# Optimization experiments

Hardware: AMD Instinct MI355X
Metric: run time of the kernel (lower is better)

Reference implementation:

```python
import jax, jax.numpy as jnp
import numpy as np

TEMPERATURE = 0.5

def setup_inputs() -> dict:
    key = jax.random.key(0)
    k1, k2 = jax.random.split(key)
    z_i = jax.random.normal(k1, (4096, 128), dtype=jnp.float32)
    z_j = jax.random.normal(k2, (4096, 128), dtype=jnp.float32)
    return {"z_i": z_i, "z_j": z_j}

def reference(z_i, z_j):
    n = z_i.shape[0]
    # L2 normalize each view (eps matches torch F.normalize default 1e-12)
    def l2norm(x):
        return x / jnp.maximum(jnp.linalg.norm(x, axis=1, keepdims=True), 1e-12)
    z = jnp.concatenate([l2norm(z_i), l2norm(z_j)], axis=0)  # [2N, D]
    sim = (z @ z.T) / TEMPERATURE                             # [2N, 2N]
    m = 2 * n
    idx = jnp.arange(m)
    pos_idx = jnp.concatenate([jnp.arange(n, m), jnp.arange(n)])  # positive pair index
    pos = sim[idx, pos_idx]                                   # [2N]
    # Per original: logits = [pos] ++ (row with diagonal removed); positive thus
    # appears twice in the logsumexp. Mask diagonal with -inf, prepend pos column.
    neg_inf = jnp.finfo(sim.dtype).min
    sim_masked = jnp.where(idx[:, None] == idx[None, :], neg_inf, sim)
    logits = jnp.concatenate([pos[:, None], sim_masked], axis=1)  # [2N, 2N+1]
    lse = jax.nn.logsumexp(logits, axis=1)
    loss = jnp.mean(lse - pos)
    return loss
```

## Files before the change

kernel.cpp:

```cpp
#include <hip/hip_runtime.h>
#include <hip/hip_bf16.h>

#define M_ROWS 8192
#define HALF_N 4096
#define D 128
#define INV_T 2.0f
#define NT 4

typedef __attribute__((ext_vector_type(4))) float f32x4;
typedef __attribute__((ext_vector_type(8))) short bf16x8;
typedef unsigned int u32;
typedef __attribute__((ext_vector_type(4))) u32 u32x4;

__global__ __launch_bounds__(256) void k_normalize(
    const float* __restrict__ zi, const float* __restrict__ zj,
    __hip_bfloat16* __restrict__ zb, float* __restrict__ rowsum)
{
    int t = blockIdx.x * 256 + threadIdx.x;
    if (t < M_ROWS) rowsum[t] = 0.0f;

    int row  = t >> 6;
    int lane = t & 63;
    const float* src = (row < HALF_N) ? (zi + (size_t)row * D)
                                      : (zj + (size_t)(row - HALF_N) * D);
    float2 v = *(const float2*)(src + lane * 2);
    float ss = v.x * v.x + v.y * v.y;
    #pragma unroll
    for (int o = 32; o >= 1; o >>= 1) ss += __shfl_xor(ss, o);
    float scale = 1.0f / fmaxf(sqrtf(ss), 1e-12f);

    __hip_bfloat162 o2;
    o2.x = __float2bfloat16(v.x * scale);
    o2.y = __float2bfloat16(v.y * scale);
    *(__hip_bfloat162*)(zb + (size_t)row * D + lane * 2) = o2;
}

__global__ __launch_bounds__(256, 2) void k_simsum(
    const __hip_bfloat16* __restrict__ zb, float* __restrict__ rowsum)
{
    __shared__ char sB[2][32768];

    const int ibase  = blockIdx.y * 128;
    const int chunk  = blockIdx.x;
    const int jbase0 = chunk * (NT * 128);
    const int tid    = threadIdx.x;
    const int wv     = tid >> 6, lane = tid & 63;
    const int lr     = lane & 15, lg = lane >> 4;
    const int rbase  = wv * 32;

    bf16x8 a[2][4];
    #pragma unroll
    for (int m = 0; m < 2; ++m)
        #pragma unroll
        for (int ks = 0; ks < 4; ++ks) {
            int row = ibase + rbase + m * 16 + lr;
            a[m][ks] = *(const bf16x8*)(zb + (size_t)row * D + (ks * 4 + lg) * 8);
        }

    u32x4 breg[8];
    auto load_tile = [&](int t) {
        int jb = jbase0 + t * 128;
        #pragma unroll
        for (int i = 0; i < 8; ++i) {
            int row = (wv * 8 + i) * 4 + lg;
            breg[i] = *(const u32x4*)(zb + (size_t)(jb + row) * D + lr * 8);
        }
    };
    auto write_tile = [&](char* buf) {
        #pragma unroll
        for (int i = 0; i < 8; ++i) {
            int row = (wv * 8 + i) * 4 + lg;
            *(u32x4*)(buf + row * 256 + ((lr ^ (row & 7)) << 4)) = breg[i];
        }
    };

    float eacc[2][4] = {{0.f, 0.f, 0.f, 0.f}, {0.f, 0.f, 0.f, 0.f}};

    load_tile(0);
    write_tile(sB[0]);
    __syncthreads();

    for (int t = 0; t < NT; ++t) {
        if (t + 1 < NT) load_tile(t + 1);
        const char* cur = sB[t & 1];

        f32x4 acc[2][8];
        #pragma unroll
        for (int m = 0; m < 2; ++m)
            #pragma unroll
            for (int n = 0; n < 8; ++n) acc[m][n] = (f32x4){0.f, 0.f, 0.f, 0.f};

        #pragma unroll
        for (int ks = 0; ks < 4; ++ks) {
            #pragma unroll
            for (int n = 0; n < 8; ++n) {
                int rowB = n * 16 + lr;
                bf16x8 b = *(const bf16x8*)(cur + rowB * 256 +
                            ((((ks << 2) + lg) ^ (lr & 7)) << 4));
                acc[0][n] = __builtin_amdgcn_mfma_f32_16x16x32_bf16(a[0][ks], b, acc[0][n], 0, 0, 0);
                acc[1][n] = __builtin_amdgcn_mfma_f32_16x16x32_bf16(a[1][ks], b, acc[1][n], 0, 0, 0);
            }
        }

        #pragma unroll
        for (int m = 0; m < 2; ++m)
            #pragma unroll
            for (int n = 0; n < 8; ++n)
                #pragma unroll
                for (int r = 0; r < 4; ++r)
                    eacc[m][r] += __expf(INV_T * acc[m][n][r]);

        __syncthreads();
        if (t + 1 < NT) {
            write_tile(sB[(t + 1) & 1]);
            __syncthreads();
        }
    }

    #pragma unroll
    for (int m = 0; m < 2; ++m)
        #pragma unroll
        for (int r = 0; r < 4; ++r) {
            float e = eacc[m][r];
            e += __shfl_xor(e, 1);
            e += __shfl_xor(e, 2);
            e += __shfl_xor(e, 4);
            e += __shfl_xor(e, 8);
            if (lr == 0)
                atomicAdd(&rowsum[ibase + rbase + m * 16 + lg * 4 + r], e);
        }
}

__global__ __launch_bounds__(256) void k_rowloss(
    const __hip_bfloat16* __restrict__ zb, const float* __restrict__ rowsum,
    float* __restrict__ rowloss)
{
    int t = blockIdx.x * 256 + threadIdx.x;
    int row = t >> 6, lane = t & 63;
    int pair = row ^ HALF_N;

    __hip_bfloat162 av = *(const __hip_bfloat162*)(zb + (size_t)row  * D + lane * 2);
    __hip_bfloat162 bv = *(const __hip_bfloat162*)(zb + (size_t)pair * D + lane * 2);
    float ax = __bfloat162float(av.x), ay = __bfloat162float(av.y);
    float bx = __bfloat162float(bv.x), by = __bfloat162float(bv.y);
    float sd = ax * ax + ay * ay;
    float pd = ax * bx + ay * by;
    #pragma unroll
    for (int o = 32; o >= 1; o >>= 1) {
        sd += __shfl_xor(sd, o);
        pd += __shfl_xor(pd, o);
    }
    if (lane == 0) {
        float rs  = rowsum[row];
        float val = rs - __expf(INV_T * sd) + __expf(INV_T * pd);
        rowloss[row] = logf(val) - INV_T * pd;
    }
}

__global__ __launch_bounds__(1024) void k_reduce(
    const float* __restrict__ rowloss, float* __restrict__ out)
{
    __shared__ float sm[16];
    int tid = threadIdx.x;
    float s = 0.f;
    #pragma unroll
    for (int i = 0; i < M_ROWS / 1024; ++i) s += rowloss[i * 1024 + tid];
    #pragma unroll
    for (int o = 32; o >= 1; o >>= 1) s += __shfl_xor(s, o);
    if ((tid & 63) == 0) sm[tid >> 6] = s;
    __syncthreads();
    if (tid == 0) {
        float tot = 0.f;
        #pragma unroll
        for (int w = 0; w < 16; ++w) tot += sm[w];
        out[0] = tot * (1.0f / (float)M_ROWS);
    }
}

extern "C" void kernel_launch(void* const* d_in, const int* in_sizes, int n_in,
                              void* d_out, int out_size, void* d_ws, size_t ws_size,
                              hipStream_t stream)
{
    const float* zi = (const float*)d_in[0];
    const float* zj = (const float*)d_in[1];

    float* rowsum  = (float*)d_ws;
    float* rowloss = rowsum + M_ROWS;
    __hip_bfloat16* zb = (__hip_bfloat16*)((char*)d_ws + 65536);

    k_normalize<<<dim3(M_ROWS * 64 / 256), 256, 0, stream>>>(zi, zj, zb, rowsum);
    k_simsum<<<dim3(16, 64), dim3(256), 0, stream>>>(zb, rowsum);
    k_rowloss<<<dim3(M_ROWS * 64 / 256), 256, 0, stream>>>(zb, rowsum, rowloss);
    k_reduce<<<dim3(1), dim3(1024), 0, stream>>>(rowloss, (float*)d_out);
}
```

Before: 38.77 us.

## Exploit similarity symmetry to compute only upper-triangular tile panels

Uses the symmetry of z·zᵀ so each block computes only tiles with column panel at or after its row panel. Column sums of the exp values are reduced through shared memory and atomically added to the column rows, which roughly halves the MFMA and exp work. The shared-memory tile buffer becomes single-buffered, and occupancy is raised to 3 blocks per SIMD. In exchange it adds extra shuffles, LDS traffic and atomics per tile, and the triangular grid leaves many blocks exiting early and others with fewer tiles, which causes load imbalance.

```diff
diff --git a/kernel.cpp b/kernel.cpp
--- a/kernel.cpp
+++ b/kernel.cpp
@@ -5,7 +5,8 @@
 #define HALF_N 4096
 #define D 128
 #define INV_T 2.0f
-#define NT 4
+#define NTC 4
+#define NPANEL 64
 
 typedef __attribute__((ext_vector_type(4))) float f32x4;
 typedef __attribute__((ext_vector_type(8))) short bf16x8;
@@ -35,18 +36,22 @@
     *(__hip_bfloat162*)(zb + (size_t)row * D + lane * 2) = o2;
 }
 
-__global__ __launch_bounds__(256, 2) void k_simsum(
+__global__ __launch_bounds__(256, 3) void k_simsum(
     const __hip_bfloat16* __restrict__ zb, float* __restrict__ rowsum)
 {
-    __shared__ char sB[2][32768];
-
-    const int ibase  = blockIdx.y * 128;
-    const int chunk  = blockIdx.x;
-    const int jbase0 = chunk * (NT * 128);
-    const int tid    = threadIdx.x;
-    const int wv     = tid >> 6, lane = tid & 63;
-    const int lr     = lane & 15, lg = lane >> 4;
-    const int rbase  = wv * 32;
+    __shared__ char  sB[32768];
+    __shared__ float colLDS[4][128];
+
+    const int pi = blockIdx.y;
+    const int j0 = pi + blockIdx.x * NTC;
+    if (j0 >= NPANEL) return;
+    const int ntiles = min(NTC, NPANEL - j0);
+
+    const int ibase = pi * 128;
+    const int tid   = threadIdx.x;
+    const int wv    = tid >> 6, lane = tid & 63;
+    const int lr    = lane & 15, lg = lane >> 4;
+    const int rbase = wv * 32;
 
     bf16x8 a[2][4];
     #pragma unroll
@@ -58,31 +63,30 @@
         }
 
     u32x4 breg[8];
-    auto load_tile = [&](int t) {
-        int jb = jbase0 + t * 128;
+    auto load_tile = [&](int pj) {
         #pragma unroll
         for (int i = 0; i < 8; ++i) {
             int row = (wv * 8 + i) * 4 + lg;
-            breg[i] = *(const u32x4*)(zb + (size_t)(jb + row) * D + lr * 8);
+            breg[i] = *(const u32x4*)(zb + (size_t)(pj * 128 + row) * D + lr * 8);
         }
     };
-    auto write_tile = [&](char* buf) {
+    auto write_tile = [&]() {
         #pragma unroll
         for (int i = 0; i < 8; ++i) {
             int row = (wv * 8 + i) * 4 + lg;
-            *(u32x4*)(buf + row * 256 + ((lr ^ (row & 7)) << 4)) = breg[i];
+            *(u32x4*)(sB + row * 256 + ((lr ^ (row & 7)) << 4)) = breg[i];
         }
     };
 
     float eacc[2][4] = {{0.f, 0.f, 0.f, 0.f}, {0.f, 0.f, 0.f, 0.f}};
 
-    load_tile(0);
-    write_tile(sB[0]);
+    load_tile(j0);
+    write_tile();
     __syncthreads();
 
-    for (int t = 0; t < NT; ++t) {
-        if (t + 1 < NT) load_tile(t + 1);
-        const char* cur = sB[t & 1];
+    for (int t = 0; t < ntiles; ++t) {
+        const int pj = j0 + t;
+        if (t + 1 < ntiles) load_tile(pj + 1);
 
         f32x4 acc[2][8];
         #pragma unroll
@@ -95,26 +99,43 @@
             #pragma unroll
             for (int n = 0; n < 8; ++n) {
                 int rowB = n * 16 + lr;
-                bf16x8 b = *(const bf16x8*)(cur + rowB * 256 +
+                bf16x8 b = *(const bf16x8*)(sB + rowB * 256 +
                             ((((ks << 2) + lg) ^ (lr & 7)) << 4));
                 acc[0][n] = __builtin_amdgcn_mfma_f32_16x16x32_bf16(a[0][ks], b, acc[0][n], 0, 0, 0);
                 acc[1][n] = __builtin_amdgcn_mfma_f32_16x16x32_bf16(a[1][ks], b, acc[1][n], 0, 0, 0);
             }
         }
 
+        float cs[8] = {0.f, 0.f, 0.f, 0.f, 0.f, 0.f, 0.f, 0.f};
         #pragma unroll
         for (int m = 0; m < 2; ++m)
             #pragma unroll
             for (int n = 0; n < 8; ++n)
                 #pragma unroll
-                for (int r = 0; r < 4; ++r)
-                    eacc[m][r] += __expf(INV_T * acc[m][n][r]);
+                for (int r = 0; r < 4; ++r) {
+                    float e = __expf(INV_T * acc[m][n][r]);
+                    eacc[m][r] += e;
+                    cs[n]      += e;
+                }
+
+        #pragma unroll
+        for (int n = 0; n < 8; ++n) {
+            cs[n] += __shfl_xor(cs[n], 16);
+            cs[n] += __shfl_xor(cs[n], 32);
+        }
+        if (lg == 0) {
+            #pragma unroll
+            for (int n = 0; n < 8; ++n) colLDS[wv][n * 16 + lr] = cs[n];
+        }
 
         __syncthreads();
-        if (t + 1 < NT) {
-            write_tile(sB[(t + 1) & 1]);
-            __syncthreads();
-        }
+        if (t + 1 < ntiles) write_tile();
+        if (pj != pi && tid < 128) {
+            float cv = colLDS[0][tid] + colLDS[1][tid] +
+                       colLDS[2][tid] + colLDS[3][tid];
+            atomicAdd(&rowsum[pj * 128 + tid], cv);
+        }
+        __syncthreads();
     }
 
     #pragma unroll
```

After: 53.19 us. +37.2%, slower.

## Replace atomic row sums with per-chunk partials and deepen the B-tile prefetch

Applied to the files above, without the earlier changes.

Each simsum block now writes its row partial sums to a per-chunk buffer instead of atomically adding, and the rowloss kernel sums the eight partials with its existing shuffle reduction. The grid is halved in x by doubling tiles per block (NT 4→8), which gives better reuse of the A fragments. The LDS pipeline now preloads two tiles ahead and writes the next tile at the top of each iteration, dropping one barrier per iteration. exp is computed as exp2f with a folded constant. Fewer blocks (512) may reduce occupancy and load balance on the GPU.

```diff
diff --git a/kernel.cpp b/kernel.cpp
--- a/kernel.cpp
+++ b/kernel.cpp
@@ -4,8 +4,9 @@
 #define M_ROWS 8192
 #define HALF_N 4096
 #define D 128
-#define INV_T 2.0f
-#define NT 4
+#define NT 8
+#define NCHUNK 8
+#define E2C 2.8853900817779268f
 
 typedef __attribute__((ext_vector_type(4))) float f32x4;
 typedef __attribute__((ext_vector_type(8))) short bf16x8;
@@ -14,11 +15,9 @@
 
 __global__ __launch_bounds__(256) void k_normalize(
     const float* __restrict__ zi, const float* __restrict__ zj,
-    __hip_bfloat16* __restrict__ zb, float* __restrict__ rowsum)
+    __hip_bfloat16* __restrict__ zb)
 {
     int t = blockIdx.x * 256 + threadIdx.x;
-    if (t < M_ROWS) rowsum[t] = 0.0f;
-
     int row  = t >> 6;
     int lane = t & 63;
     const float* src = (row < HALF_N) ? (zi + (size_t)row * D)
@@ -36,17 +35,18 @@
 }
 
 __global__ __launch_bounds__(256, 2) void k_simsum(
-    const __hip_bfloat16* __restrict__ zb, float* __restrict__ rowsum)
+    const __hip_bfloat16* __restrict__ zb, float* __restrict__ rspart)
 {
     __shared__ char sB[2][32768];
 
-    const int ibase  = blockIdx.y * 128;
-    const int chunk  = blockIdx.x;
-    const int jbase0 = chunk * (NT * 128);
-    const int tid    = threadIdx.x;
-    const int wv     = tid >> 6, lane = tid & 63;
-    const int lr     = lane & 15, lg = lane >> 4;
-    const int rbase  = wv * 32;
+    const int chunk = blockIdx.x;
+    const int pi    = blockIdx.y;
+    const int ibase = pi * 128;
+    const int jbase = chunk * (NT * 128);
+    const int tid   = threadIdx.x;
+    const int wv    = tid >> 6, lane = tid & 63;
+    const int lr    = lane & 15, lg = lane >> 4;
+    const int rbase = wv * 32;
 
     bf16x8 a[2][4];
     #pragma unroll
@@ -59,11 +59,11 @@
 
     u32x4 breg[8];
     auto load_tile = [&](int t) {
-        int jb = jbase0 + t * 128;
+        const __hip_bfloat16* src = zb + (size_t)(jbase + t * 128) * D;
         #pragma unroll
         for (int i = 0; i < 8; ++i) {
             int row = (wv * 8 + i) * 4 + lg;
-            breg[i] = *(const u32x4*)(zb + (size_t)(jb + row) * D + lr * 8);
+            breg[i] = *(const u32x4*)(src + (size_t)row * D + lr * 8);
         }
     };
     auto write_tile = [&](char* buf) {
@@ -78,12 +78,14 @@
 
     load_tile(0);
     write_tile(sB[0]);
+    load_tile(1);
     __syncthreads();
 
     for (int t = 0; t < NT; ++t) {
-        if (t + 1 < NT) load_tile(t + 1);
+        if (t + 1 < NT) write_tile(sB[(t + 1) & 1]);
+        if (t + 2 < NT) load_tile(t + 2);
+
         const char* cur = sB[t & 1];
-
         f32x4 acc[2][8];
         #pragma unroll
         for (int m = 0; m < 2; ++m)
@@ -95,10 +97,10 @@
             #pragma unroll
             for (int n = 0; n < 8; ++n) {
                 int rowB = n * 16 + lr;
-                bf16x8 b = *(const bf16x8*)(cur + rowB * 256 +
-                            ((((ks << 2) + lg) ^ (lr & 7)) << 4));
-                acc[0][n] = __builtin_amdgcn_mfma_f32_16x16x32_bf16(a[0][ks], b, acc[0][n], 0, 0, 0);
-                acc[1][n] = __builtin_amdgcn_mfma_f32_16x16x32_bf16(a[1][ks], b, acc[1][n], 0, 0, 0);
+                bf16x8 bfr = *(const bf16x8*)(cur + rowB * 256 +
+                              ((((ks << 2) + lg) ^ (lr & 7)) << 4));
+                acc[0][n] = __builtin_amdgcn_mfma_f32_16x16x32_bf16(a[0][ks], bfr, acc[0][n], 0, 0, 0);
+                acc[1][n] = __builtin_amdgcn_mfma_f32_16x16x32_bf16(a[1][ks], bfr, acc[1][n], 0, 0, 0);
             }
         }
 
@@ -108,13 +110,9 @@
             for (int n = 0; n < 8; ++n)
                 #pragma unroll
                 for (int r = 0; r < 4; ++r)
-                    eacc[m][r] += __expf(INV_T * acc[m][n][r]);
+                    eacc[m][r] += exp2f(acc[m][n][r] * E2C);
 
         __syncthreads();
-        if (t + 1 < NT) {
-            write_tile(sB[(t + 1) & 1]);
-            __syncthreads();
-        }
     }
 
     #pragma unroll
@@ -127,17 +125,19 @@
             e += __shfl_xor(e, 4);
             e += __shfl_xor(e, 8);
             if (lr == 0)
-                atomicAdd(&rowsum[ibase + rbase + m * 16 + lg * 4 + r], e);
+                rspart[chunk * M_ROWS + ibase + rbase + m * 16 + lg * 4 + r] = e;
         }
 }
 
 __global__ __launch_bounds__(256) void k_rowloss(
-    const __hip_bfloat16* __restrict__ zb, const float* __restrict__ rowsum,
+    const __hip_bfloat16* __restrict__ zb, const float* __restrict__ rspart,
     float* __restrict__ rowloss)
 {
     int t = blockIdx.x * 256 + threadIdx.x;
     int row = t >> 6, lane = t & 63;
     int pair = row ^ HALF_N;
+
+    float rs = (lane < NCHUNK) ? rspart[lane * M_ROWS + row] : 0.f;
 
     __hip_bfloat162 av = *(const __hip_bfloat162*)(zb + (size_t)row  * D + lane * 2);
     __hip_bfloat162 bv = *(const __hip_bfloat162*)(zb + (size_t)pair * D + lane * 2);
@@ -149,11 +149,11 @@
     for (int o = 32; o >= 1; o >>= 1) {
         sd += __shfl_xor(sd, o);
         pd += __shfl_xor(pd, o);
+        rs += __shfl_xor(rs, o);
     }
     if (lane == 0) {
-        float rs  = rowsum[row];
-        float val = rs - __expf(INV_T * sd) + __expf(INV_T * pd);
-        rowloss[row] = logf(val) - INV_T * pd;
+        float val = rs - exp2f(sd * E2C) + exp2f(pd * E2C);
+        rowloss[row] = logf(val) - 2.0f * pd;
     }
 }
 
@@ -184,12 +184,12 @@
     const float* zi = (const float*)d_in[0];
     const float* zj = (const float*)d_in[1];
 
-    float* rowsum  = (float*)d_ws;
-    float* rowloss = rowsum + M_ROWS;
-    __hip_bfloat16* zb = (__hip_bfloat16*)((char*)d_ws + 65536);
+    float* rspart  = (float*)d_ws;
+    float* rowloss = (float*)((char*)d_ws + 262144);
+    __hip_bfloat16* zb = (__hip_bfloat16*)((char*)d_ws + 262144 + 32768);
 
-    k_normalize<<<dim3(M_ROWS * 64 / 256), 256, 0, stream>>>(zi, zj, zb, rowsum);
-    k_simsum<<<dim3(16, 64), dim3(256), 0, stream>>>(zb, rowsum);
-    k_rowloss<<<dim3(M_ROWS * 64 / 256), 256, 0, stream>>>(zb, rowsum, rowloss);
+    k_normalize<<<dim3(M_ROWS * 64 / 256), 256, 0, stream>>>(zi, zj, zb);
+    k_simsum<<<dim3(NCHUNK, 64), dim3(256), 0, stream>>>(zb, rspart);
+    k_rowloss<<<dim3(M_ROWS * 64 / 256), 256, 0, stream>>>(zb, rspart, rowloss);
     k_reduce<<<dim3(1), dim3(1024), 0, stream>>>(rowloss, (float*)d_out);
 }
```

Measured after the change: 45.05 us. 1.16x slower.
